# Optimization experiments

Measured on AMD Instinct MI355X. Metric: run time of the kernel, lower is better.

The kernel has to match this reference:

```python
import jax, jax.numpy as jnp
import numpy as np

B, LQ, LK, D, H = 4, 1024, 2048, 1024, 16
DH = D // H  # 64
EPS = 1e-6
ROPE_BASE = 10000.0


def _rms_norm(x, w):
    # RMSNorm over last dim (d_head)
    var = jnp.mean(jnp.square(x), axis=-1, keepdims=True)
    return x * jax.lax.rsqrt(var + EPS) * w


def _rope(x, pos):
    # x: [B,H,L,dh], pos: [L] int. Half-split rotation.
    half = x.shape[-1] // 2
    inv_freq = ROPE_BASE ** (-jnp.arange(0, half, dtype=jnp.float32) / half)
    ang = pos.astype(jnp.float32)[:, None] * inv_freq  # [L, half]
    cos, sin = jnp.cos(ang), jnp.sin(ang)              # [L, half]
    x1, x2 = x[..., :half], x[..., half:]
    return jnp.concatenate([x1 * cos - x2 * sin, x1 * sin + x2 * cos], axis=-1)


def setup_inputs() -> dict:
    key = jax.random.key(0)
    ks = jax.random.split(key, 7)
    s = 1.0 / np.sqrt(D)
    return {
        "queries": jax.random.normal(ks[0], (B, LQ, D), jnp.float32),
        "kv": jax.random.normal(ks[1], (B, LK, D), jnp.float32),
        "wq": jax.random.normal(ks[2], (D, D), jnp.float32) * s,
        "wkv": jax.random.normal(ks[3], (2 * D, D), jnp.float32) * s,
        "wo": jax.random.normal(ks[4], (D, D), jnp.float32) * s,
        "q_norm_w": jnp.ones((DH,), jnp.float32),
        "k_norm_w": jnp.ones((DH,), jnp.float32),
        "pos_q": jnp.arange(LQ, dtype=jnp.int32),
        "pos_k": jnp.arange(LK, dtype=jnp.int32),
    }


def reference(queries, kv, wq, wkv, wo, q_norm_w, k_norm_w, pos_q, pos_k):
    b, lq, d = queries.shape
    lk = kv.shape[1]
    scale = DH ** -0.5
    # projections (torch Linear: x @ W.T)
    q = (queries @ wq.T).reshape(b, lq, H, DH).transpose(0, 2, 1, 3)  # [B,H,Lq,dh]
    kvp = (kv @ wkv.T).reshape(b, lk, H, 2 * DH).transpose(0, 2, 1, 3)
    k, v = kvp[..., :DH], kvp[..., DH:]                               # [B,H,Lk,dh]
    q = _rms_norm(q, q_norm_w)
    k = _rms_norm(k, k_norm_w)
    q = _rope(q, pos_q)
    k = _rope(k, pos_k)
    scores = jnp.einsum("bhqd,bhkd->bhqk", q, k) * scale
    attn = jax.nn.softmax(scores, axis=-1)
    y = jnp.einsum("bhqk,bhkd->bhqd", attn, v)        # [B,H,Lq,dh]
    y = y.transpose(0, 2, 1, 3).reshape(b, lq, d)     # [B,Lq,D]
    return y @ wo.T
```

## Files before the change

kernel.cpp:

```cpp
#include <hip/hip_runtime.h>
#include <stdint.h>

typedef unsigned short u16;
typedef u16 u16x8 __attribute__((ext_vector_type(8)));
typedef u16 u16x4 __attribute__((ext_vector_type(4)));
typedef short s16x8 __attribute__((ext_vector_type(8)));
typedef float f32x4 __attribute__((ext_vector_type(4)));

#define B_ 4
#define LQ_ 1024
#define LK_ 2048
#define D_ 1024
#define H_ 16
#define DH_ 64
#define QSCL 0.1803368801111204f
#define L2_10000 13.287712379549449f

__device__ __forceinline__ u16 f2bf(float x) {
  uint32_t u = __float_as_uint(x);
  u += 0x7FFFu + ((u >> 16) & 1u);
  return (u16)(u >> 16);
}
__device__ __forceinline__ float bf2f(u16 h) {
  return __uint_as_float(((uint32_t)h) << 16);
}
__device__ __forceinline__ uint32_t cvtpk(float lo, float hi) {
  uint32_t r;
  asm("v_cvt_pk_bf16_f32 %0, %1, %2" : "=v"(r) : "v"(lo), "v"(hi));
  return r;
}
__device__ __forceinline__ float exp2fast(float x) {
  float r;
  asm("v_exp_f32 %0, %1" : "=v"(r) : "v"(x));
  return r;
}

__global__ __launch_bounds__(256) void cast5_k(const float* __restrict__ s0, u16* __restrict__ d0,
                                               const float* __restrict__ s1, u16* __restrict__ d1,
                                               const float* __restrict__ s2, u16* __restrict__ d2,
                                               const float* __restrict__ s3, u16* __restrict__ d3,
                                               const float* __restrict__ s4, u16* __restrict__ d4) {
  int b = blockIdx.x;
  const float* s;
  u16* d;
  int base;
  if (b < 4096) { s = s0; d = d0; base = b; }
  else if (b < 5120) { s = s1; d = d1; base = b - 4096; }
  else if (b < 13312) { s = s2; d = d2; base = b - 5120; }
  else if (b < 15360) { s = s3; d = d3; base = b - 13312; }
  else { s = s4; d = d4; base = b - 15360; }
  int i = (base * 256 + threadIdx.x) * 4;
  float4 v = *(const float4*)(s + i);
  ushort4 o;
  o.x = f2bf(v.x); o.y = f2bf(v.y); o.z = f2bf(v.z); o.w = f2bf(v.w);
  *(ushort4*)(d + i) = o;
}

__global__ __launch_bounds__(256) void gemm_bt(const u16* __restrict__ A,
                                               const u16* __restrict__ Bm,
                                               float* __restrict__ C,
                                               int N) {
  __shared__ __align__(16) u16 As[2][128 * 32];
  __shared__ __align__(16) u16 Bs[2][128 * 32];
  const int tid = threadIdx.x;
  const int lane = tid & 63;
  const int wid = tid >> 6;
  const int m0 = blockIdx.x * 128;
  const int n0 = blockIdx.y * 128;
  const int slice = 1024 / gridDim.z;
  const int kStart = blockIdx.z * slice;
  const int NT = slice >> 5;
  C += (size_t)blockIdx.z * (size_t)gridDim.x * 128 * N;
  const int wr = (wid >> 1) * 64;
  const int wc = (wid & 1) * 64;
  const int fr = lane & 15;
  const int fq = lane >> 4;
  const int srow = lane >> 2;
  const int schunk = lane & 3;

  f32x4 zero = {0.f, 0.f, 0.f, 0.f};
  f32x4 acc[4][4];
  for (int i = 0; i < 4; i++)
    for (int j = 0; j < 4; j++) acc[i][j] = zero;

  const int r0 = wid * 32;
  const u16* gA = A + (size_t)(m0 + r0 + srow) * 1024 + schunk * 8;
  const u16* gB = Bm + (size_t)(n0 + r0 + srow) * 1024 + schunk * 8;

  auto stage = [&](int buf, int k0) {
    u16* lA = &As[buf][r0 * 32];
    u16* lB = &Bs[buf][r0 * 32];
    __builtin_amdgcn_global_load_lds(
        (const __attribute__((address_space(1))) void*)(gA + k0),
        (__attribute__((address_space(3))) void*)(lA), 16, 0, 0);
    __builtin_amdgcn_global_load_lds(
        (const __attribute__((address_space(1))) void*)(gA + k0 + (size_t)16 * 1024),
        (__attribute__((address_space(3))) void*)(lA + 16 * 32), 16, 0, 0);
    __builtin_amdgcn_global_load_lds(
        (const __attribute__((address_space(1))) void*)(gB + k0),
        (__attribute__((address_space(3))) void*)(lB), 16, 0, 0);
    __builtin_amdgcn_global_load_lds(
        (const __attribute__((address_space(1))) void*)(gB + k0 + (size_t)16 * 1024),
        (__attribute__((address_space(3))) void*)(lB + 16 * 32), 16, 0, 0);
  };

  stage(0, kStart);
  stage(1, kStart + 32);
  asm volatile("s_waitcnt vmcnt(4)" ::: "memory");
  __builtin_amdgcn_s_barrier();

  for (int t = 0; t < NT; t++) {
    const int cur = t & 1;
    s16x8 af[4], bf[4];
#pragma unroll
    for (int mi = 0; mi < 4; mi++)
      af[mi] = *(const s16x8*)&As[cur][(wr + mi * 16 + fr) * 32 + fq * 8];
#pragma unroll
    for (int ni = 0; ni < 4; ni++)
      bf[ni] = *(const s16x8*)&Bs[cur][(wc + ni * 16 + fr) * 32 + fq * 8];
#pragma unroll
    for (int mi = 0; mi < 4; mi++)
#pragma unroll
      for (int ni = 0; ni < 4; ni++)
        acc[mi][ni] = __builtin_amdgcn_mfma_f32_16x16x32_bf16(af[mi], bf[ni],
                                                              acc[mi][ni], 0, 0, 0);
    __builtin_amdgcn_s_barrier();
    if (t + 2 < NT) {
      stage(cur, kStart + (t + 2) * 32);
      asm volatile("s_waitcnt vmcnt(4)" ::: "memory");
    } else {
      asm volatile("s_waitcnt vmcnt(0)" ::: "memory");
    }
    __builtin_amdgcn_s_barrier();
  }
#pragma unroll
  for (int mi = 0; mi < 4; mi++) {
#pragma unroll
    for (int ni = 0; ni < 4; ni++) {
      int row = m0 + wr + mi * 16 + fq * 4;
      int col = n0 + wc + ni * 16 + fr;
#pragma unroll
      for (int r = 0; r < 4; r++) C[(size_t)(row + r) * N + col] = acc[mi][ni][r];
    }
  }
}

#define BAR8 asm volatile("s_barrier" ::: "memory")
__global__ __launch_bounds__(512, 2) void gemm_bt256(const u16* __restrict__ A,
                                                     const u16* __restrict__ Bm,
                                                     u16* __restrict__ C) {
  __shared__ __align__(16) u16 lds[65536];
  const int N = 2048;
  const int tid = threadIdx.x;
  const int lane = tid & 63;
  const int w = tid >> 6;
  const int wr = w >> 2;
  const int wc = w & 3;
  const int fr = lane & 15;
  const int fq = lane >> 4;
  const int nwg = gridDim.x;
  const int cpx = nwg >> 3;
  const int bid = blockIdx.x;
  const int swz = (bid & 7) * cpx + (bid >> 3);
  const int nbn = N >> 8;
  const int bm = swz / nbn, bn = swz % nbn;
  const int gm0 = bm * 256, gn0 = bn * 256;
  const int NT = 16;

  f32x4 zero = {0.f, 0.f, 0.f, 0.f};
  f32x4 acc[8][4];
#pragma unroll
  for (int i = 0; i < 8; i++)
#pragma unroll
    for (int j = 0; j < 4; j++) acc[i][j] = zero;

  auto stage = [&](int buf, int t, int s) {
    int q = (s & 3) * 512 + tid;
    int row = q >> 3, p = q & 7;
    int l = p ^ (row & 7);
    const u16* src = (s < 4)
        ? A + (size_t)(gm0 + row) * 1024 + (t << 6) + l * 8
        : Bm + (size_t)(gn0 + row) * 1024 + (t << 6) + l * 8;
    u16* dst = &lds[buf * 32768 + ((s < 4) ? 0 : 16384) + ((s & 3) * 512 + w * 64) * 8];
    __builtin_amdgcn_global_load_lds(
        (const __attribute__((address_space(1))) void*)src,
        (__attribute__((address_space(3))) void*)dst, 16, 0, 0);
  };
  auto rdA = [&](int buf, int mi, int kk) -> s16x8 {
    int row = wr * 128 + mi * 16 + fr;
    int l = (kk * 4 + fq) ^ (fr & 7);
    return *(const s16x8*)&lds[buf * 32768 + row * 64 + l * 8];
  };
  auto rdB = [&](int buf, int ni, int kk) -> s16x8 {
    int row = wc * 64 + ni * 16 + fr;
    int l = (kk * 4 + fq) ^ (fr & 7);
    return *(const s16x8*)&lds[buf * 32768 + 16384 + row * 64 + l * 8];
  };

  s16x8 af[4][2], bf[4][2];

#pragma unroll
  for (int s = 4; s < 8; s++) stage(0, 0, s);
#pragma unroll
  for (int s = 0; s < 4; s++) stage(0, 0, s);
#pragma unroll
  for (int s = 4; s < 8; s++) stage(1, 1, s);
#pragma unroll
  for (int s = 0; s < 4; s++) stage(1, 1, s);
  asm volatile("s_waitcnt vmcnt(8)" ::: "memory");
  BAR8;

  for (int t = 0; t < NT; t++) {
    const int cur = t & 1;
    const bool st2 = (t + 2 < NT);
#pragma unroll
    for (int mi = 0; mi < 4; mi++)
#pragma unroll
      for (int kk = 0; kk < 2; kk++) af[mi][kk] = rdA(cur, mi, kk);
#pragma unroll
    for (int ni = 0; ni < 2; ni++)
#pragma unroll
      for (int kk = 0; kk < 2; kk++) bf[ni][kk] = rdB(cur, ni, kk);
    BAR8;
    __builtin_amdgcn_s_setprio(1);
#pragma unroll
    for (int mi = 0; mi < 4; mi++)
#pragma unroll
      for (int ni = 0; ni < 2; ni++)
#pragma unroll
        for (int kk = 0; kk < 2; kk++)
          acc[mi][ni] = __builtin_amdgcn_mfma_f32_16x16x32_bf16(af[mi][kk], bf[ni][kk],
                                                                acc[mi][ni], 0, 0, 0);
    __builtin_amdgcn_s_setprio(0);
    BAR8;
#pragma unroll
    for (int ni = 2; ni < 4; ni++)
#pragma unroll
      for (int kk = 0; kk < 2; kk++) bf[ni][kk] = rdB(cur, ni, kk);
    BAR8;
    __builtin_amdgcn_s_setprio(1);
#pragma unroll
    for (int mi = 0; mi < 4; mi++)
#pragma unroll
      for (int ni = 2; ni < 4; ni++)
#pragma unroll
        for (int kk = 0; kk < 2; kk++)
          acc[mi][ni] = __builtin_amdgcn_mfma_f32_16x16x32_bf16(af[mi][kk], bf[ni][kk],
                                                                acc[mi][ni], 0, 0, 0);
    __builtin_amdgcn_s_setprio(0);
    BAR8;
#pragma unroll
    for (int mi = 0; mi < 4; mi++)
#pragma unroll
      for (int kk = 0; kk < 2; kk++) af[mi][kk] = rdA(cur, mi + 4, kk);
    if (st2) {
#pragma unroll
      for (int s = 4; s < 8; s++) stage(cur, t + 2, s);
    }
    BAR8;
    __builtin_amdgcn_s_setprio(1);
#pragma unroll
    for (int mi = 0; mi < 4; mi++)
#pragma unroll
      for (int ni = 2; ni < 4; ni++)
#pragma unroll
        for (int kk = 0; kk < 2; kk++)
          acc[mi + 4][ni] = __builtin_amdgcn_mfma_f32_16x16x32_bf16(
              af[mi][kk], bf[ni][kk], acc[mi + 4][ni], 0, 0, 0);
    __builtin_amdgcn_s_setprio(0);
    BAR8;
    if (st2) {
#pragma unroll
      for (int s = 0; s < 4; s++) stage(cur, t + 2, s);
      asm volatile("s_waitcnt vmcnt(8)" ::: "memory");
    } else {
      asm volatile("s_waitcnt vmcnt(0)" ::: "memory");
    }
    BAR8;
    __builtin_amdgcn_s_setprio(1);
#pragma unroll
    for (int mi = 0; mi < 4; mi++)
#pragma unroll
      for (int ni = 0; ni < 2; ni++)
#pragma unroll
        for (int kk = 0; kk < 2; kk++)
          acc[mi + 4][ni] = __builtin_amdgcn_mfma_f32_16x16x32_bf16(
              af[mi][kk], bf[ni][kk], acc[mi + 4][ni], 0, 0, 0);
    __builtin_amdgcn_s_setprio(0);
    BAR8;
  }
#pragma unroll
  for (int mi = 0; mi < 8; mi++) {
#pragma unroll
    for (int ni = 0; ni < 4; ni++) {
      int row = gm0 + wr * 128 + mi * 16 + fq * 4;
      int col = gn0 + wc * 64 + ni * 16 + fr;
#pragma unroll
      for (int r = 0; r < 4; r++) C[(size_t)(row + r) * N + col] = f2bf(acc[mi][ni][r]);
    }
  }
}

__global__ __launch_bounds__(256) void norm_rope_q(const float* __restrict__ src,
                                                   size_t partStride,
                                                   const float* __restrict__ w,
                                                   const int* __restrict__ pos,
                                                   u16* __restrict__ dst) {
  int wid = threadIdx.x >> 6;
  int lane = threadIdx.x & 63;
  int g = blockIdx.x * 4 + wid;
  int h = g & 15;
  int bl = g >> 4;
  int b = bl >> 10;
  int l = bl & 1023;
  size_t idx = (size_t)bl * 1024 + h * 64 + lane;
  float x = src[idx] + src[partStride + idx];
  float ss = x * x;
#pragma unroll
  for (int m = 1; m < 64; m <<= 1) ss += __shfl_xor(ss, m, 64);
  float xn = x * rsqrtf(ss * (1.0f / 64.0f) + 1e-6f) * w[lane];
  float p = __shfl_xor(xn, 32, 64);
  int j = lane & 31;
  float freq = exp2fast(-(float)j * (L2_10000 / 32.f));
  float ang = (float)pos[l] * freq;
  float c = cosf(ang), s = sinf(ang);
  float o = (lane < 32) ? (xn * c - p * s) : (p * s + xn * c);
  dst[((size_t)(b * 16 + h) * 1024 + l) * 64 + lane] = f2bf(o * QSCL);
}

__global__ __launch_bounds__(256) void normv_k(const u16* __restrict__ src,
                                               const float* __restrict__ w,
                                               const int* __restrict__ pos,
                                               u16* __restrict__ Kb,
                                               u16* __restrict__ Vt) {
  __shared__ u16 tile[64][66];
  int kt = blockIdx.x & 31;
  int bh = blockIdx.x >> 5;
  int h = bh & 15;
  int b = bh >> 4;
  int c = threadIdx.x & 63;
  int r4 = threadIdx.x >> 6;
  const u16* ksrc = src + ((size_t)(b * LK_ + kt * 64)) * 2048 + h * 128;
  u16* kdst = Kb + ((size_t)bh * LK_ + kt * 64) * 64;
  float wn = w[c];
  float freq = exp2fast(-(float)(c & 31) * (L2_10000 / 32.f));
#pragma unroll
  for (int p = 0; p < 16; p++) {
    int lk = p * 4 + r4;
    float x = bf2f(ksrc[(size_t)lk * 2048 + c]);
    float ss = x * x;
#pragma unroll
    for (int m = 1; m < 64; m <<= 1) ss += __shfl_xor(ss, m, 64);
    float xn = x * rsqrtf(ss * (1.0f / 64.0f) + 1e-6f) * wn;
    float pv = __shfl_xor(xn, 32, 64);
    float ang = (float)pos[kt * 64 + lk] * freq;
    float cc = cosf(ang), s = sinf(ang);
    float o = (c < 32) ? (xn * cc - pv * s) : (pv * s + xn * cc);
    kdst[(size_t)lk * 64 + c] = f2bf(o);
  }
  const u16* vsrc = ksrc + 64;
#pragma unroll
  for (int p = 0; p < 16; p++) {
    int lk = p * 4 + r4;
    tile[lk][c] = vsrc[(size_t)lk * 2048 + c];
  }
  __syncthreads();
  u16* vdst = Vt + (size_t)bh * 64 * LK_ + kt * 64;
#pragma unroll
  for (int p = 0; p < 16; p++) {
    int dh = p * 4 + r4;
    vdst[(size_t)dh * LK_ + c] = tile[c][dh];
  }
}

__global__ __launch_bounds__(256) void reduce2_k(const float* __restrict__ p,
                                                 float* __restrict__ out, int n) {
  int i = (blockIdx.x * 256 + threadIdx.x) * 4;
  if (i >= n) return;
  float4 a = *(const float4*)(p + i);
  float4 b = *(const float4*)(p + (size_t)n + i);
  float4 r = make_float4(a.x + b.x, a.y + b.y, a.z + b.z, a.w + b.w);
  *(float4*)(out + i) = r;
}

__global__ __launch_bounds__(256) void flash_k(const u16* __restrict__ qb,
                                               const u16* __restrict__ kb,
                                               const u16* __restrict__ vb,
                                               u16* __restrict__ y1) {
  __shared__ __align__(16) u16 Ks[2][64][64];
  __shared__ __align__(16) u16 Vs[2][64][64];
  const int tid = threadIdx.x;
  const int lane = tid & 63;
  const int wid = tid >> 6;
  const int fr = lane & 15;
  const int fq = lane >> 4;
  int bid = blockIdx.x;
  int vbid = (bid & 7) * 64 + (bid >> 3);
  int qt = vbid & 7;
  int bh = vbid >> 3;
  const u16* qbase = qb + ((size_t)bh * LQ_ + qt * 128 + wid * 32) * 64;
  const u16* kbase = kb + (size_t)bh * LK_ * 64;
  const u16* vbase = vb + (size_t)bh * 64 * LK_;
  s16x8 qf0a = *(const s16x8*)(qbase + (size_t)fr * 64 + fq * 8);
  s16x8 qf1a = *(const s16x8*)(qbase + (size_t)fr * 64 + 32 + fq * 8);
  s16x8 qf0b = *(const s16x8*)(qbase + (size_t)(16 + fr) * 64 + fq * 8);
  s16x8 qf1b = *(const s16x8*)(qbase + (size_t)(16 + fr) * 64 + 32 + fq * 8);
  s16x8 ones;
#pragma unroll
  for (int e = 0; e < 8; e++) ones[e] = (short)0x3F80;
  float mrunA = -1e30f, mrunB = -1e30f;
  f32x4 zero = {0.f, 0.f, 0.f, 0.f};
  f32x4 yaccA[4], yaccB[4], yonesA = zero, yonesB = zero;
#pragma unroll
  for (int ni = 0; ni < 4; ni++) { yaccA[ni] = zero; yaccB[ni] = zero; }
  const int srow = tid >> 3;
  const int schunk = tid & 7;
  const int c2 = schunk >> 2, c1 = (schunk >> 1) & 1, c0 = schunk & 1;
  const int vg1 = 4 * c2 + 2 * c0;
  const int voff = 4 * c1;

  auto kaddr = [&](int bufi, int row) -> u16* {
    return &Ks[bufi][row][(schunk ^ (row & 7)) << 3];
  };
  auto stageV = [&](int bufi, int row, u16x8 v) {
    u16x4 lo4 = __builtin_shufflevector(v, v, 0, 1, 2, 3);
    u16x4 hi4 = __builtin_shufflevector(v, v, 4, 5, 6, 7);
    *(u16x4*)&Vs[bufi][row][((vg1 ^ (row & 7)) << 3) + voff] = lo4;
    *(u16x4*)&Vs[bufi][row][(((vg1 + 1) ^ (row & 7)) << 3) + voff] = hi4;
  };
  auto qk2 = [&](int bufi, f32x4 (&sA)[4], f32x4 (&sB)[4]) {
#pragma unroll
    for (int ni = 0; ni < 4; ni++) { sA[ni] = zero; sB[ni] = zero; }
#pragma unroll
    for (int ni = 0; ni < 4; ni++) {
      int row = ni * 16 + fr;
      s16x8 kf0 = *(const s16x8*)&Ks[bufi][row][(fq ^ (fr & 7)) << 3];
      s16x8 kf1 = *(const s16x8*)&Ks[bufi][row][((4 + fq) ^ (fr & 7)) << 3];
      sA[ni] = __builtin_amdgcn_mfma_f32_16x16x32_bf16(kf0, qf0a, sA[ni], 0, 0, 0);
      sA[ni] = __builtin_amdgcn_mfma_f32_16x16x32_bf16(kf1, qf1a, sA[ni], 0, 0, 0);
      sB[ni] = __builtin_amdgcn_mfma_f32_16x16x32_bf16(kf0, qf0b, sB[ni], 0, 0, 0);
      sB[ni] = __builtin_amdgcn_mfma_f32_16x16x32_bf16(kf1, qf1b, sB[ni], 0, 0, 0);
    }
  };
  auto softmax = [&](f32x4 (&sp)[4], float& mrun, f32x4 (&yacc)[4], f32x4& yones) {
    float m0 = fmaxf(fmaxf(sp[0][0], sp[0][1]), sp[0][2]);
    float m1 = fmaxf(fmaxf(sp[0][3], sp[1][0]), sp[1][1]);
    float m2 = fmaxf(fmaxf(sp[1][2], sp[1][3]), sp[2][0]);
    float m3 = fmaxf(fmaxf(sp[2][1], sp[2][2]), sp[2][3]);
    float m4 = fmaxf(fmaxf(sp[3][0], sp[3][1]), sp[3][2]);
    float mx = fmaxf(fmaxf(fmaxf(m0, m1), m2), fmaxf(fmaxf(m3, m4), sp[3][3]));
    mx = fmaxf(mx, __shfl_xor(mx, 16, 64));
    mx = fmaxf(mx, __shfl_xor(mx, 32, 64));
    bool skip = __all(mx <= mrun + 10.0f);
    if (!skip) {
      float mn = fmaxf(mrun, mx);
      float alpha = exp2fast(mrun - mn);
      mrun = mn;
      float va[4];
#pragma unroll
      for (int r = 0; r < 4; r++) va[r] = __shfl(alpha, fq * 4 + r, 64);
#pragma unroll
      for (int ni = 0; ni < 4; ni++)
#pragma unroll
        for (int r = 0; r < 4; r++) yacc[ni][r] *= va[r];
#pragma unroll
      for (int r = 0; r < 4; r++) yones[r] *= va[r];
    }
#pragma unroll
    for (int ni = 0; ni < 4; ni++)
#pragma unroll
      for (int r = 0; r < 4; r++) sp[ni][r] = exp2fast(sp[ni][r] - mrun);
  };

  const int NT = LK_ / 64;
  f32x4 spA[4], spB[4], snA[4], snB[4];

  {
    u16x8 k0 = *(const u16x8*)(kbase + (size_t)srow * 64 + schunk * 8);
    u16x8 k1 = *(const u16x8*)(kbase + (size_t)(srow + 32) * 64 + schunk * 8);
    u16x8 v0 = *(const u16x8*)(vbase + (size_t)srow * LK_ + schunk * 8);
    u16x8 v1 = *(const u16x8*)(vbase + (size_t)(srow + 32) * LK_ + schunk * 8);
    *(u16x8*)kaddr(0, srow) = k0;
    *(u16x8*)kaddr(0, srow + 32) = k1;
    stageV(0, srow, v0);
    stageV(0, srow + 32, v1);
    __syncthreads();
    u16x8 ka = *(const u16x8*)(kbase + (size_t)(64 + srow) * 64 + schunk * 8);
    u16x8 kb2 = *(const u16x8*)(kbase + (size_t)(64 + srow + 32) * 64 + schunk * 8);
    u16x8 va = *(const u16x8*)(vbase + (size_t)srow * LK_ + 64 + schunk * 8);
    u16x8 vb2 = *(const u16x8*)(vbase + (size_t)(srow + 32) * LK_ + 64 + schunk * 8);
    *(u16x8*)kaddr(1, srow) = ka;
    *(u16x8*)kaddr(1, srow + 32) = kb2;
    stageV(1, srow, va);
    stageV(1, srow + 32, vb2);
    qk2(0, spA, spB);
    __syncthreads();
  }

  const u16* kp0 = kbase + (size_t)(128 + srow) * 64 + schunk * 8;
  const u16* kp1 = kbase + (size_t)(128 + srow + 32) * 64 + schunk * 8;
  const u16* vp0 = vbase + (size_t)srow * LK_ + 128 + schunk * 8;
  const u16* vp1 = vbase + (size_t)(srow + 32) * LK_ + 128 + schunk * 8;

  for (int t = 0; t < NT; t++) {
    const int cur = t & 1;
    const bool st2 = (t + 2 < NT);
    u16x8 kr0 = *(const u16x8*)kp0;
    u16x8 kr1 = *(const u16x8*)kp1;
    u16x8 vr0 = *(const u16x8*)vp0;
    u16x8 vr1 = *(const u16x8*)vp1;
    kp0 += 64 * 64; kp1 += 64 * 64;
    vp0 += 64; vp1 += 64;
    if (t + 1 < NT) qk2(cur ^ 1, snA, snB);
    softmax(spA, mrunA, yaccA, yonesA);
    softmax(spB, mrunB, yaccB, yonesB);
#pragma unroll
    for (int s2 = 0; s2 < 2; s2++) {
      union { uint32_t u[4]; s16x8 v8; } puA, puB;
      puA.u[0] = cvtpk(spA[2 * s2][0], spA[2 * s2][1]);
      puA.u[1] = cvtpk(spA[2 * s2][2], spA[2 * s2][3]);
      puA.u[2] = cvtpk(spA[2 * s2 + 1][0], spA[2 * s2 + 1][1]);
      puA.u[3] = cvtpk(spA[2 * s2 + 1][2], spA[2 * s2 + 1][3]);
      puB.u[0] = cvtpk(spB[2 * s2][0], spB[2 * s2][1]);
      puB.u[1] = cvtpk(spB[2 * s2][2], spB[2 * s2][3]);
      puB.u[2] = cvtpk(spB[2 * s2 + 1][0], spB[2 * s2 + 1][1]);
      puB.u[3] = cvtpk(spB[2 * s2 + 1][2], spB[2 * s2 + 1][3]);
#pragma unroll
      for (int ni = 0; ni < 4; ni++) {
        int row = ni * 16 + fr;
        s16x8 vf = *(const s16x8*)&Vs[cur][row][(((4 * s2 + fq) ^ (fr & 7)) << 3)];
        yaccA[ni] = __builtin_amdgcn_mfma_f32_16x16x32_bf16(puA.v8, vf, yaccA[ni], 0, 0, 0);
        yaccB[ni] = __builtin_amdgcn_mfma_f32_16x16x32_bf16(puB.v8, vf, yaccB[ni], 0, 0, 0);
      }
      yonesA = __builtin_amdgcn_mfma_f32_16x16x32_bf16(puA.v8, ones, yonesA, 0, 0, 0);
      yonesB = __builtin_amdgcn_mfma_f32_16x16x32_bf16(puB.v8, ones, yonesB, 0, 0, 0);
    }
    __syncthreads();
    if (st2) {
      *(u16x8*)kaddr(cur, srow) = kr0;
      *(u16x8*)kaddr(cur, srow + 32) = kr1;
      stageV(cur, srow, vr0);
      stageV(cur, srow + 32, vr1);
    }
    __syncthreads();
#pragma unroll
    for (int ni = 0; ni < 4; ni++) { spA[ni] = snA[ni]; spB[ni] = snB[ni]; }
  }
  int b = bh >> 4, h = bh & 15;
  u16* yoA = y1 + ((size_t)(b * LQ_ + qt * 128 + wid * 32 + fq * 4)) * 1024 + h * 64;
  u16* yoB = yoA + (size_t)16 * 1024;
#pragma unroll
  for (int ni = 0; ni < 4; ni++) {
#pragma unroll
    for (int r = 0; r < 4; r++) {
      yoA[(size_t)r * 1024 + ni * 16 + fr] = f2bf(yaccA[ni][r] / yonesA[r]);
      yoB[(size_t)r * 1024 + ni * 16 + fr] = f2bf(yaccB[ni][r] / yonesB[r]);
    }
  }
}

extern "C" void kernel_launch(void* const* d_in, const int* in_sizes, int n_in,
                              void* d_out, int out_size, void* d_ws, size_t ws_size,
                              hipStream_t stream) {
  (void)in_sizes; (void)n_in; (void)out_size;
  const float* queries = (const float*)d_in[0];
  const float* kv = (const float*)d_in[1];
  const float* wq = (const float*)d_in[2];
  const float* wkv = (const float*)d_in[3];
  const float* wo = (const float*)d_in[4];
  const float* qnw = (const float*)d_in[5];
  const float* knw = (const float*)d_in[6];
  const int* pos_q = (const int*)d_in[7];
  const int* pos_k = (const int*)d_in[8];
  float* out = (float*)d_out;

  char* ws = (char*)d_ws;
  size_t off = 0;
  auto alloc = [&](size_t sz) { void* p = ws + off; off += sz; return p; };
  u16* Aq1 = (u16*)alloc((size_t)4096 * 1024 * 2);
  u16* Wqh = (u16*)alloc((size_t)1024 * 1024 * 2);
  u16* Akv1 = (u16*)alloc((size_t)8192 * 1024 * 2);
  u16* Wkvh = (u16*)alloc((size_t)2048 * 1024 * 2);
  u16* Woh = (u16*)alloc((size_t)1024 * 1024 * 2);
  u16* KVp = (u16*)alloc((size_t)8192 * 2048 * 2);
  u16* Qb = (u16*)alloc((size_t)64 * 1024 * 64 * 2);
  u16* Kb = (u16*)alloc((size_t)64 * 2048 * 64 * 2 + 32768);
  u16* Vt = (u16*)alloc((size_t)64 * 2048 * 64 * 2 + 32768);
  u16* Y1 = (u16*)alloc((size_t)4096 * 1024 * 2);
  float* Part = (float*)alloc((size_t)2 * 4096 * 1024 * 4);
  if (off > ws_size) return;

  const size_t PSTRIDE = (size_t)4096 * 1024;

  cast5_k<<<16384, 256, 0, stream>>>(queries, Aq1, wq, Wqh, kv, Akv1, wkv, Wkvh, wo, Woh);
  gemm_bt256<<<(8192 / 256) * (2048 / 256), 512, 0, stream>>>(Akv1, Wkvh, KVp);
  gemm_bt<<<dim3(4096 / 128, 1024 / 128, 2), 256, 0, stream>>>(Aq1, Wqh, Part, 1024);
  norm_rope_q<<<4096 * 16 / 4, 256, 0, stream>>>(Part, PSTRIDE, qnw, pos_q, Qb);
  normv_k<<<64 * 32, 256, 0, stream>>>(KVp, knw, pos_k, Kb, Vt);
  flash_k<<<64 * 8, 256, 0, stream>>>(Qb, Kb, Vt, Y1);
  gemm_bt<<<dim3(4096 / 128, 1024 / 128, 2), 256, 0, stream>>>(Y1, Woh, Part, 1024);
  reduce2_k<<<4096, 256, 0, stream>>>(Part, out, 4096 * 1024);
}
```

Measured before the change: 192.9 us.

## Split flash attention over KV into two halves and merge partials

The attention kernel now splits the key/value sequence into two halves, doubling the grid from 512 to 1024 blocks. Each block writes an unnormalized bf16 partial output plus its running max and row sum, and a new merge kernel combines the two halves with log-sum-exp rescaling. The aim is better occupancy of the GPU's compute units, since 512 blocks may underfill the device. In exchange it adds an extra launch, extra global traffic for the partials, and bf16 rounding of unnormalized accumulators.

```diff
diff --git a/kernel.cpp b/kernel.cpp
--- a/kernel.cpp
+++ b/kernel.cpp
@@ -386,7 +386,9 @@
 __global__ __launch_bounds__(256) void flash_k(const u16* __restrict__ qb,
                                                const u16* __restrict__ kb,
                                                const u16* __restrict__ vb,
-                                               u16* __restrict__ y1) {
+                                               u16* __restrict__ yp,
+                                               float* __restrict__ lp,
+                                               float* __restrict__ mp) {
   __shared__ __align__(16) u16 Ks[2][64][64];
   __shared__ __align__(16) u16 Vs[2][64][64];
   const int tid = threadIdx.x;
@@ -395,12 +397,14 @@
   const int fr = lane & 15;
   const int fq = lane >> 4;
   int bid = blockIdx.x;
-  int vbid = (bid & 7) * 64 + (bid >> 3);
-  int qt = vbid & 7;
-  int bh = vbid >> 3;
+  int vbid = (bid & 7) * 128 + (bid >> 3);
+  int kvs = vbid >> 9;
+  int rem = vbid & 511;
+  int qt = rem & 7;
+  int bh = rem >> 3;
   const u16* qbase = qb + ((size_t)bh * LQ_ + qt * 128 + wid * 32) * 64;
-  const u16* kbase = kb + (size_t)bh * LK_ * 64;
-  const u16* vbase = vb + (size_t)bh * 64 * LK_;
+  const u16* kbase = kb + ((size_t)bh * LK_ + kvs * 1024) * 64;
+  const u16* vbase = vb + (size_t)bh * 64 * LK_ + kvs * 1024;
   s16x8 qf0a = *(const s16x8*)(qbase + (size_t)fr * 64 + fq * 8);
   s16x8 qf1a = *(const s16x8*)(qbase + (size_t)fr * 64 + 32 + fq * 8);
   s16x8 qf0b = *(const s16x8*)(qbase + (size_t)(16 + fr) * 64 + fq * 8);
@@ -472,7 +476,7 @@
       for (int r = 0; r < 4; r++) sp[ni][r] = exp2fast(sp[ni][r] - mrun);
   };
 
-  const int NT = LK_ / 64;
+  const int NT = 16;
   f32x4 spA[4], spB[4], snA[4], snB[4];
 
   {
@@ -546,17 +550,66 @@
 #pragma unroll
     for (int ni = 0; ni < 4; ni++) { spA[ni] = snA[ni]; spB[ni] = snB[ni]; }
   }
+  const int pbh = kvs * 64 + bh;
+  const int ql0 = qt * 128 + wid * 32;
+  u16* ypA = yp + ((size_t)pbh * 1024 + ql0 + fq * 4) * 64;
+  u16* ypB = ypA + (size_t)16 * 64;
+#pragma unroll
+  for (int ni = 0; ni < 4; ni++) {
+#pragma unroll
+    for (int r = 0; r < 4; r++) {
+      ypA[(size_t)r * 64 + ni * 16 + fr] = f2bf(yaccA[ni][r]);
+      ypB[(size_t)r * 64 + ni * 16 + fr] = f2bf(yaccB[ni][r]);
+    }
+  }
+  if (fr == 0) {
+    float* lA = lp + (size_t)pbh * 1024 + ql0 + fq * 4;
+#pragma unroll
+    for (int r = 0; r < 4; r++) {
+      lA[r] = yonesA[r];
+      lA[16 + r] = yonesB[r];
+    }
+  }
+  if (fq == 0) {
+    float* mA = mp + (size_t)pbh * 1024 + ql0;
+    mA[fr] = mrunA;
+    mA[16 + fr] = mrunB;
+  }
+}
+
+__global__ __launch_bounds__(256) void merge_k(const u16* __restrict__ yp,
+                                               const float* __restrict__ lp,
+                                               const float* __restrict__ mp,
+                                               u16* __restrict__ y1) {
+  int blk = blockIdx.x;
+  int bh = blk >> 4;
+  int chunk = blk & 15;
+  int row = chunk * 64 + (threadIdx.x >> 2);
+  int dhg = (threadIdx.x & 3) * 16;
+  size_t i0 = (size_t)bh * 1024 + row;
+  size_t i1 = (size_t)(64 + bh) * 1024 + row;
+  float m0 = mp[i0], m1 = mp[i1];
+  float l0 = lp[i0], l1 = lp[i1];
+  float mm = fmaxf(m0, m1);
+  float a0 = exp2fast(m0 - mm), a1 = exp2fast(m1 - mm);
+  float s = 1.0f / (l0 * a0 + l1 * a1);
+  float s0 = a0 * s, s1 = a1 * s;
+  const u16* y0p = yp + i0 * 64 + dhg;
+  const u16* y1p = yp + i1 * 64 + dhg;
   int b = bh >> 4, h = bh & 15;
-  u16* yoA = y1 + ((size_t)(b * LQ_ + qt * 128 + wid * 32 + fq * 4)) * 1024 + h * 64;
-  u16* yoB = yoA + (size_t)16 * 1024;
-#pragma unroll
-  for (int ni = 0; ni < 4; ni++) {
-#pragma unroll
-    for (int r = 0; r < 4; r++) {
-      yoA[(size_t)r * 1024 + ni * 16 + fr] = f2bf(yaccA[ni][r] / yonesA[r]);
-      yoB[(size_t)r * 1024 + ni * 16 + fr] = f2bf(yaccB[ni][r] / yonesB[r]);
-    }
-  }
+  u16* od = y1 + ((size_t)(b * 1024 + row)) * 1024 + h * 64 + dhg;
+  u16x8 r0a = *(const u16x8*)y0p;
+  u16x8 r0b = *(const u16x8*)(y0p + 8);
+  u16x8 r1a = *(const u16x8*)y1p;
+  u16x8 r1b = *(const u16x8*)(y1p + 8);
+  u16x8 oa, ob;
+#pragma unroll
+  for (int e = 0; e < 8; e++) {
+    oa[e] = f2bf(bf2f(r0a[e]) * s0 + bf2f(r1a[e]) * s1);
+    ob[e] = f2bf(bf2f(r0b[e]) * s0 + bf2f(r1b[e]) * s1);
+  }
+  *(u16x8*)od = oa;
+  *(u16x8*)(od + 8) = ob;
 }
 
 extern "C" void kernel_launch(void* const* d_in, const int* in_sizes, int n_in,
@@ -587,6 +640,9 @@
   u16* Kb = (u16*)alloc((size_t)64 * 2048 * 64 * 2 + 32768);
   u16* Vt = (u16*)alloc((size_t)64 * 2048 * 64 * 2 + 32768);
   u16* Y1 = (u16*)alloc((size_t)4096 * 1024 * 2);
+  u16* Yp = (u16*)alloc((size_t)2 * 64 * 1024 * 64 * 2);
+  float* Lp = (float*)alloc((size_t)2 * 64 * 1024 * 4);
+  float* Mp = (float*)alloc((size_t)2 * 64 * 1024 * 4);
   float* Part = (float*)alloc((size_t)2 * 4096 * 1024 * 4);
   if (off > ws_size) return;
 
@@ -597,7 +653,8 @@
   gemm_bt<<<dim3(4096 / 128, 1024 / 128, 2), 256, 0, stream>>>(Aq1, Wqh, Part, 1024);
   norm_rope_q<<<4096 * 16 / 4, 256, 0, stream>>>(Part, PSTRIDE, qnw, pos_q, Qb);
   normv_k<<<64 * 32, 256, 0, stream>>>(KVp, knw, pos_k, Kb, Vt);
-  flash_k<<<64 * 8, 256, 0, stream>>>(Qb, Kb, Vt, Y1);
+  flash_k<<<1024, 256, 0, stream>>>(Qb, Kb, Vt, Yp, Lp, Mp);
+  merge_k<<<1024, 256, 0, stream>>>(Yp, Lp, Mp, Y1);
   gemm_bt<<<dim3(4096 / 128, 1024 / 128, 2), 256, 0, stream>>>(Y1, Woh, Part, 1024);
   reduce2_k<<<4096, 256, 0, stream>>>(Part, out, 4096 * 1024);
 }
```

Measured after the change: 198.4 us. 1.03x slower.

## Load K and V fragments directly from global memory, dropping LDS staging

Applied to the files above, without the earlier changes.

The flash attention kernel no longer stages K/V tiles through double-buffered shared memory with __syncthreads. Each wave now reads its MFMA K fragments and V fragments straight from global memory (relying on L1/L2 for reuse across the 4 waves), which removes the barriers and LDS traffic. In exchange it issues more and less coalesced global loads (V is read as 8-byte pieces per lane), and the loads are no longer prefetched a tile ahead, so memory latency may be exposed.

```diff
diff --git a/kernel.cpp b/kernel.cpp
--- a/kernel.cpp
+++ b/kernel.cpp
@@ -387,8 +387,6 @@
                                                const u16* __restrict__ kb,
                                                const u16* __restrict__ vb,
                                                u16* __restrict__ y1) {
-  __shared__ __align__(16) u16 Ks[2][64][64];
-  __shared__ __align__(16) u16 Vs[2][64][64];
   const int tid = threadIdx.x;
   const int lane = tid & 63;
   const int wid = tid >> 6;
@@ -399,8 +397,8 @@
   int qt = vbid & 7;
   int bh = vbid >> 3;
   const u16* qbase = qb + ((size_t)bh * LQ_ + qt * 128 + wid * 32) * 64;
-  const u16* kbase = kb + (size_t)bh * LK_ * 64;
-  const u16* vbase = vb + (size_t)bh * 64 * LK_;
+  const u16* kp = kb + (size_t)bh * LK_ * 64 + (size_t)fr * 64 + fq * 8;
+  const u16* vpb = vb + (size_t)bh * 64 * LK_ + (size_t)fr * LK_;
   s16x8 qf0a = *(const s16x8*)(qbase + (size_t)fr * 64 + fq * 8);
   s16x8 qf1a = *(const s16x8*)(qbase + (size_t)fr * 64 + 32 + fq * 8);
   s16x8 qf0b = *(const s16x8*)(qbase + (size_t)(16 + fr) * 64 + fq * 8);
@@ -413,33 +411,23 @@
   f32x4 yaccA[4], yaccB[4], yonesA = zero, yonesB = zero;
 #pragma unroll
   for (int ni = 0; ni < 4; ni++) { yaccA[ni] = zero; yaccB[ni] = zero; }
-  const int srow = tid >> 3;
-  const int schunk = tid & 7;
-  const int c2 = schunk >> 2, c1 = (schunk >> 1) & 1, c0 = schunk & 1;
-  const int vg1 = 4 * c2 + 2 * c0;
-  const int voff = 4 * c1;
-
-  auto kaddr = [&](int bufi, int row) -> u16* {
-    return &Ks[bufi][row][(schunk ^ (row & 7)) << 3];
-  };
-  auto stageV = [&](int bufi, int row, u16x8 v) {
-    u16x4 lo4 = __builtin_shufflevector(v, v, 0, 1, 2, 3);
-    u16x4 hi4 = __builtin_shufflevector(v, v, 4, 5, 6, 7);
-    *(u16x4*)&Vs[bufi][row][((vg1 ^ (row & 7)) << 3) + voff] = lo4;
-    *(u16x4*)&Vs[bufi][row][(((vg1 + 1) ^ (row & 7)) << 3) + voff] = hi4;
-  };
-  auto qk2 = [&](int bufi, f32x4 (&sA)[4], f32x4 (&sB)[4]) {
+
+  auto qk2 = [&](int t, f32x4 (&sA)[4], f32x4 (&sB)[4]) {
+    const u16* kt = kp + (size_t)t * 4096;
+    s16x8 kf0[4], kf1[4];
+#pragma unroll
+    for (int ni = 0; ni < 4; ni++) {
+      kf0[ni] = *(const s16x8*)(kt + ni * 1024);
+      kf1[ni] = *(const s16x8*)(kt + ni * 1024 + 32);
+    }
 #pragma unroll
     for (int ni = 0; ni < 4; ni++) { sA[ni] = zero; sB[ni] = zero; }
 #pragma unroll
     for (int ni = 0; ni < 4; ni++) {
-      int row = ni * 16 + fr;
-      s16x8 kf0 = *(const s16x8*)&Ks[bufi][row][(fq ^ (fr & 7)) << 3];
-      s16x8 kf1 = *(const s16x8*)&Ks[bufi][row][((4 + fq) ^ (fr & 7)) << 3];
-      sA[ni] = __builtin_amdgcn_mfma_f32_16x16x32_bf16(kf0, qf0a, sA[ni], 0, 0, 0);
-      sA[ni] = __builtin_amdgcn_mfma_f32_16x16x32_bf16(kf1, qf1a, sA[ni], 0, 0, 0);
-      sB[ni] = __builtin_amdgcn_mfma_f32_16x16x32_bf16(kf0, qf0b, sB[ni], 0, 0, 0);
-      sB[ni] = __builtin_amdgcn_mfma_f32_16x16x32_bf16(kf1, qf1b, sB[ni], 0, 0, 0);
+      sA[ni] = __builtin_amdgcn_mfma_f32_16x16x32_bf16(kf0[ni], qf0a, sA[ni], 0, 0, 0);
+      sA[ni] = __builtin_amdgcn_mfma_f32_16x16x32_bf16(kf1[ni], qf1a, sA[ni], 0, 0, 0);
+      sB[ni] = __builtin_amdgcn_mfma_f32_16x16x32_bf16(kf0[ni], qf0b, sB[ni], 0, 0, 0);
+      sB[ni] = __builtin_amdgcn_mfma_f32_16x16x32_bf16(kf1[ni], qf1b, sB[ni], 0, 0, 0);
     }
   };
   auto softmax = [&](f32x4 (&sp)[4], float& mrun, f32x4 (&yacc)[4], f32x4& yones) {
@@ -471,78 +459,44 @@
 #pragma unroll
       for (int r = 0; r < 4; r++) sp[ni][r] = exp2fast(sp[ni][r] - mrun);
   };
-
-  const int NT = LK_ / 64;
-  f32x4 spA[4], spB[4], snA[4], snB[4];
-
-  {
-    u16x8 k0 = *(const u16x8*)(kbase + (size_t)srow * 64 + schunk * 8);
-    u16x8 k1 = *(const u16x8*)(kbase + (size_t)(srow + 32) * 64 + schunk * 8);
-    u16x8 v0 = *(const u16x8*)(vbase + (size_t)srow * LK_ + schunk * 8);
-    u16x8 v1 = *(const u16x8*)(vbase + (size_t)(srow + 32) * LK_ + schunk * 8);
-    *(u16x8*)kaddr(0, srow) = k0;
-    *(u16x8*)kaddr(0, srow + 32) = k1;
-    stageV(0, srow, v0);
-    stageV(0, srow + 32, v1);
-    __syncthreads();
-    u16x8 ka = *(const u16x8*)(kbase + (size_t)(64 + srow) * 64 + schunk * 8);
-    u16x8 kb2 = *(const u16x8*)(kbase + (size_t)(64 + srow + 32) * 64 + schunk * 8);
-    u16x8 va = *(const u16x8*)(vbase + (size_t)srow * LK_ + 64 + schunk * 8);
-    u16x8 vb2 = *(const u16x8*)(vbase + (size_t)(srow + 32) * LK_ + 64 + schunk * 8);
-    *(u16x8*)kaddr(1, srow) = ka;
-    *(u16x8*)kaddr(1, srow + 32) = kb2;
-    stageV(1, srow, va);
-    stageV(1, srow + 32, vb2);
-    qk2(0, spA, spB);
-    __syncthreads();
-  }
-
-  const u16* kp0 = kbase + (size_t)(128 + srow) * 64 + schunk * 8;
-  const u16* kp1 = kbase + (size_t)(128 + srow + 32) * 64 + schunk * 8;
-  const u16* vp0 = vbase + (size_t)srow * LK_ + 128 + schunk * 8;
-  const u16* vp1 = vbase + (size_t)(srow + 32) * LK_ + 128 + schunk * 8;
-
-  for (int t = 0; t < NT; t++) {
-    const int cur = t & 1;
-    const bool st2 = (t + 2 < NT);
-    u16x8 kr0 = *(const u16x8*)kp0;
-    u16x8 kr1 = *(const u16x8*)kp1;
-    u16x8 vr0 = *(const u16x8*)vp0;
-    u16x8 vr1 = *(const u16x8*)vp1;
-    kp0 += 64 * 64; kp1 += 64 * 64;
-    vp0 += 64; vp1 += 64;
-    if (t + 1 < NT) qk2(cur ^ 1, snA, snB);
-    softmax(spA, mrunA, yaccA, yonesA);
-    softmax(spB, mrunB, yaccB, yonesB);
+  auto pv = [&](int t, f32x4 (&sA)[4], f32x4 (&sB)[4]) {
+    const u16* vt = vpb + t * 64;
 #pragma unroll
     for (int s2 = 0; s2 < 2; s2++) {
       union { uint32_t u[4]; s16x8 v8; } puA, puB;
-      puA.u[0] = cvtpk(spA[2 * s2][0], spA[2 * s2][1]);
-      puA.u[1] = cvtpk(spA[2 * s2][2], spA[2 * s2][3]);
-      puA.u[2] = cvtpk(spA[2 * s2 + 1][0], spA[2 * s2 + 1][1]);
-      puA.u[3] = cvtpk(spA[2 * s2 + 1][2], spA[2 * s2 + 1][3]);
-      puB.u[0] = cvtpk(spB[2 * s2][0], spB[2 * s2][1]);
-      puB.u[1] = cvtpk(spB[2 * s2][2], spB[2 * s2][3]);
-      puB.u[2] = cvtpk(spB[2 * s2 + 1][0], spB[2 * s2 + 1][1]);
-      puB.u[3] = cvtpk(spB[2 * s2 + 1][2], spB[2 * s2 + 1][3]);
+      puA.u[0] = cvtpk(sA[2 * s2][0], sA[2 * s2][1]);
+      puA.u[1] = cvtpk(sA[2 * s2][2], sA[2 * s2][3]);
+      puA.u[2] = cvtpk(sA[2 * s2 + 1][0], sA[2 * s2 + 1][1]);
+      puA.u[3] = cvtpk(sA[2 * s2 + 1][2], sA[2 * s2 + 1][3]);
+      puB.u[0] = cvtpk(sB[2 * s2][0], sB[2 * s2][1]);
+      puB.u[1] = cvtpk(sB[2 * s2][2], sB[2 * s2][3]);
+      puB.u[2] = cvtpk(sB[2 * s2 + 1][0], sB[2 * s2 + 1][1]);
+      puB.u[3] = cvtpk(sB[2 * s2 + 1][2], sB[2 * s2 + 1][3]);
 #pragma unroll
       for (int ni = 0; ni < 4; ni++) {
-        int row = ni * 16 + fr;
-        s16x8 vf = *(const s16x8*)&Vs[cur][row][(((4 * s2 + fq) ^ (fr & 7)) << 3)];
-        yaccA[ni] = __builtin_amdgcn_mfma_f32_16x16x32_bf16(puA.v8, vf, yaccA[ni], 0, 0, 0);
-        yaccB[ni] = __builtin_amdgcn_mfma_f32_16x16x32_bf16(puB.v8, vf, yaccB[ni], 0, 0, 0);
+        const u16* vr = vt + (size_t)ni * 16 * LK_ + s2 * 32 + fq * 4;
+        u16x4 lo = *(const u16x4*)(vr);
+        u16x4 hi = *(const u16x4*)(vr + 16);
+        union { u16 h[8]; s16x8 v8; } vf;
+#pragma unroll
+        for (int e = 0; e < 4; e++) { vf.h[e] = lo[e]; vf.h[4 + e] = hi[e]; }
+        yaccA[ni] = __builtin_amdgcn_mfma_f32_16x16x32_bf16(puA.v8, vf.v8, yaccA[ni], 0, 0, 0);
+        yaccB[ni] = __builtin_amdgcn_mfma_f32_16x16x32_bf16(puB.v8, vf.v8, yaccB[ni], 0, 0, 0);
       }
       yonesA = __builtin_amdgcn_mfma_f32_16x16x32_bf16(puA.v8, ones, yonesA, 0, 0, 0);
       yonesB = __builtin_amdgcn_mfma_f32_16x16x32_bf16(puB.v8, ones, yonesB, 0, 0, 0);
     }
-    __syncthreads();
-    if (st2) {
-      *(u16x8*)kaddr(cur, srow) = kr0;
-      *(u16x8*)kaddr(cur, srow + 32) = kr1;
-      stageV(cur, srow, vr0);
-      stageV(cur, srow + 32, vr1);
-    }
-    __syncthreads();
+  };
+
+  const int NT = LK_ / 64;
+  f32x4 spA[4], spB[4], snA[4], snB[4];
+
+  qk2(0, spA, spB);
+  for (int t = 0; t < NT; t++) {
+    if (t + 1 < NT) qk2(t + 1, snA, snB);
+    softmax(spA, mrunA, yaccA, yonesA);
+    softmax(spB, mrunB, yaccB, yonesB);
+    pv(t, spA, spB);
 #pragma unroll
     for (int ni = 0; ni < 4; ni++) { spA[ni] = snA[ni]; spB[ni] = snB[ni]; }
   }
```

Result: slower. 312.6 us (+62.1%).
